# Kernel tuning notes

Measured on AMD Instinct MI355X. Metric: run time of the kernel, lower is better.

## Reference

```python
import jax, jax.numpy as jnp
import numpy as np

B, N, D, P = 16, 128, 1024, 128  # batch, seq_len, n_in, n_mlp
SCALE = 0  # scores divided by P**SCALE (supar convention); scale=0 => no-op


def setup_inputs() -> dict:
    key = jax.random.key(0)
    ks = jax.random.split(key, 6)
    s_in = 1.0 / np.sqrt(D)   # keep MLP activations ~unit scale
    s_w = 1.0 / P             # keep triple-product scores bounded
    return {
        "x": jax.random.normal(ks[0], (B, N, D), jnp.float32),
        "x_span": jax.random.normal(ks[1], (B, N, D), jnp.float32),
        # MLP projections (Linear weight stored torch-style as (out, in))
        "Wx": jax.random.normal(ks[2], (P, D), jnp.float32) * s_in,
        "bx": jnp.zeros((P,), jnp.float32),
        "Wy": jax.random.normal(ks[3], (P, D), jnp.float32) * s_in,
        "by": jnp.zeros((P,), jnp.float32),
        "Wz": jax.random.normal(ks[4], (P, D), jnp.float32) * s_in,
        "bz": jnp.zeros((P,), jnp.float32),
        # Triaffine weight: (P+1 [bias_x], P [z, no bias], P+1 [bias_y]), n_out=1 squeezed
        "W3": jax.random.normal(ks[5], (P + 1, P, P + 1), jnp.float32) * s_w,
    }


def _mlp(h, W, b):
    # supar MLP: Linear + LeakyReLU(0.1); dropout=0 at inference
    return jax.nn.leaky_relu(h @ W.T + b, 0.1)


def reference(x, x_span, Wx, bx, Wy, by, Wz, bz, W3):
    xp = _mlp(x_span, Wx, bx)  # (B,N,P)  -> triaffine arg x
    yp = _mlp(x_span, Wy, by)  # (B,N,P)  -> triaffine arg y
    zp = _mlp(x, Wz, bz)       # (B,N,P)  -> triaffine arg z (head words)
    ones = jnp.ones((B, N, 1), xp.dtype)
    x1 = jnp.concatenate([xp, ones], axis=-1)  # bias_x
    y1 = jnp.concatenate([yp, ones], axis=-1)  # bias_y
    # w: per-head-word bilinear map, (B,N,P+1,P+1)
    w = jnp.einsum('bzk,ikj->bzij', zp, W3)
    # s: (B, z, x, y) = (B,N,N,N)
    s = jnp.einsum('bxi,bzij,byj->bzxy', x1, w, y1)
    s = s / (P ** SCALE)
    # Span2oScorer: s.permute(0, 2, 3, 1).float() -> (B, span_i, span_j, head)
    return jnp.transpose(s, (0, 2, 3, 1)).astype(jnp.float32)
```

## Files before the change

### kernel.cpp

```cpp
#include <hip/hip_runtime.h>

typedef __bf16 bf16;
typedef __bf16 bf16x8 __attribute__((ext_vector_type(8)));
typedef __bf16 bf16x4 __attribute__((ext_vector_type(4)));
typedef float f32x4 __attribute__((ext_vector_type(4)));

#define MFMA(a, b, c) __builtin_amdgcn_mfma_f32_16x16x32_bf16((a), (b), (c), 0, 0, 0)

static __device__ __forceinline__ f32x4 zero4() {
    f32x4 z; z[0] = 0.f; z[1] = 0.f; z[2] = 0.f; z[3] = 0.f; return z;
}

__global__ __launch_bounds__(256) void k_prep(
    const float* __restrict__ x, const float* __restrict__ xsp,
    const float* __restrict__ Wx, const float* __restrict__ Wy, const float* __restrict__ Wz,
    const float* __restrict__ W3,
    bf16* __restrict__ xb, bf16* __restrict__ xspb, bf16* __restrict__ wbf,
    bf16* __restrict__ w3b, float* __restrict__ w3bias)
{
    const int b = blockIdx.x, t = threadIdx.x;
    if (b < 1120) {
        const float* src; bf16* dst; int base;
        if (b < 512)       { src = xsp; dst = xspb; base = b * 4096; }
        else if (b < 1024) { src = x;   dst = xb;   base = (b - 512) * 4096; }
        else {
            int i = b - 1024;
            int proj = i >> 5;
            src = (proj == 0) ? Wx : (proj == 1) ? Wy : Wz;
            dst = wbf + proj * 131072;
            base = (i & 31) * 4096;
        }
        int o = base + t * 16;
#pragma unroll
        for (int u = 0; u < 4; u++) {
            float4 v = *(const float4*)(src + o + u * 4);
            bf16x4 w; w[0] = (bf16)v.x; w[1] = (bf16)v.y; w[2] = (bf16)v.z; w[3] = (bf16)v.w;
            *(bf16x4*)(dst + o + u * 4) = w;
        }
    } else {
        int nb = b - 1120;
        int n = nb * 8 + (t >> 5);
        int c = t & 31;
        const float* row = W3 + n * 129;
        bf16x4 w;
        w[0] = (bf16)row[4 * c + 0];
        w[1] = (bf16)row[4 * c + 1];
        w[2] = (bf16)row[4 * c + 2];
        w[3] = (bf16)row[4 * c + 3];
        *(bf16x4*)(w3b + n * 136 + 4 * c) = w;
        if (c == 0) w3bias[n] = row[128];
    }
}

__global__ __launch_bounds__(256) void k_mlp(
    const bf16* __restrict__ xspb, const bf16* __restrict__ xb,
    const bf16* __restrict__ wbf,
    const float* __restrict__ bx, const float* __restrict__ by, const float* __restrict__ bz,
    bf16* __restrict__ pout)
{
    const int proj = blockIdx.y;
    const bf16* A = (proj == 2) ? xb : xspb;
    const bf16* W = wbf + proj * 131072;
    const float* bias = (proj == 0) ? bx : (proj == 1) ? by : bz;
    bf16* out = pout + proj * 262144;

    const int tid = threadIdx.x;
    const int wv = tid >> 6, lane = tid & 63, quad = lane >> 4, lr = lane & 15;
    const int m0 = blockIdx.x * 16;

    f32x4 acc[2];
    acc[0] = zero4(); acc[1] = zero4();

    const bf16* brow = A + (m0 + lr) * 1024 + quad * 8;
    const bf16* arow = W + (wv * 16 + lr) * 1024 + quad * 8;

#pragma unroll 4
    for (int kw = 0; kw < 32; kw++) {
        bf16x8 bfr = *(const bf16x8*)(brow + kw * 32);
        bf16x8 a0 = *(const bf16x8*)(arow + kw * 32);
        bf16x8 a1 = *(const bf16x8*)(arow + 65536 + kw * 32);
        acc[0] = MFMA(a0, bfr, acc[0]);
        acc[1] = MFMA(a1, bfr, acc[1]);
    }
#pragma unroll
    for (int s = 0; s < 2; s++) {
        int p = (wv + s * 4) * 16 + quad * 4;
        float4 bv = *(const float4*)(bias + p);
        int m = m0 + lr;
        bf16x4 o;
        float v0 = acc[s][0] + bv.x; o[0] = (bf16)(v0 > 0.f ? v0 : 0.1f * v0);
        float v1 = acc[s][1] + bv.y; o[1] = (bf16)(v1 > 0.f ? v1 : 0.1f * v1);
        float v2 = acc[s][2] + bv.z; o[2] = (bf16)(v2 > 0.f ? v2 : 0.1f * v2);
        float v3 = acc[s][3] + bv.w; o[3] = (bf16)(v3 > 0.f ? v3 : 0.1f * v3);
        *(bf16x4*)(out + m * 128 + p) = o;
    }
}

__global__ __launch_bounds__(256, 4) void k_vgemm(
    const bf16* __restrict__ yp,
    const bf16* __restrict__ w3b,
    const float* __restrict__ w3bias,
    bf16* __restrict__ V)
{
    __shared__ bf16 Vt[128 * 136];
    const int b = blockIdx.y;
    const int n0 = blockIdx.x * 128;
    const int tid = threadIdx.x;
    const int wv = tid >> 6, lane = tid & 63, quad = lane >> 4, lr = lane & 15;
    const int y0 = wv * 32;

    const bf16* Ab = yp + b * 16384;

    f32x4 acc[8][2];
#pragma unroll
    for (int nt = 0; nt < 8; nt++) { acc[nt][0] = zero4(); acc[nt][1] = zero4(); }

#pragma unroll
    for (int kw = 0; kw < 4; kw++) {
        bf16x8 b0 = *(const bf16x8*)(Ab + (y0 + lr) * 128 + kw * 32 + quad * 8);
        bf16x8 b1 = *(const bf16x8*)(Ab + (y0 + 16 + lr) * 128 + kw * 32 + quad * 8);
#pragma unroll
        for (int nt = 0; nt < 8; nt++) {
            bf16x8 af = *(const bf16x8*)(w3b + (n0 + nt * 16 + lr) * 136 + kw * 32 + quad * 8);
            acc[nt][0] = MFMA(af, b0, acc[nt][0]);
            acc[nt][1] = MFMA(af, b1, acc[nt][1]);
        }
    }
#pragma unroll
    for (int nt = 0; nt < 8; nt++) {
        int nl = nt * 16 + quad * 4;
        float4 bv = *(const float4*)(w3bias + n0 + nl);
#pragma unroll
        for (int s = 0; s < 2; s++) {
            int y = y0 + s * 16 + lr;
            bf16x4 o;
            o[0] = (bf16)(acc[nt][s][0] + bv.x);
            o[1] = (bf16)(acc[nt][s][1] + bv.y);
            o[2] = (bf16)(acc[nt][s][2] + bv.z);
            o[3] = (bf16)(acc[nt][s][3] + bv.w);
            *(bf16x4*)(&Vt[y * 136 + nl]) = o;
        }
    }
    __syncthreads();
    const int yr = tid >> 4, nn = (tid & 15) * 8;
#pragma unroll
    for (int pass = 0; pass < 8; pass++) {
        int y = pass * 16 + yr;
        bf16x8 v = *(const bf16x8*)(&Vt[y * 136 + nn]);
        *(bf16x8*)(V + (b * 128 + y) * 16512 + n0 + nn) = v;
    }
}

__global__ __launch_bounds__(512, 4) void k_score(
    const bf16* __restrict__ xp,
    const bf16* __restrict__ zp,
    const bf16* __restrict__ V,
    float* __restrict__ out)
{
    __shared__ __align__(16) bf16 Vl[129 * 136];
    __shared__ float Hb[128];
    const int bi = blockIdx.x;
    const int b = bi >> 7, y = bi & 127;
    const int tid = threadIdx.x;
    const int wv = tid >> 6, lane = tid & 63, quad = lane >> 4, lr = lane & 15;
    const int r0 = wv * 16 + lr;

    const bf16* Zb = zp + b * 16384;
    const bf16* Xb = xp + b * 16384;
    const bf16* Vby = V + (b * 128 + y) * 16512;

    bf16x8 st[4];
#pragma unroll
    for (int u = 0; u < 4; u++) st[u] = *(const bf16x8*)(Vby + (tid + u * 512) * 8);
    bf16x8 st4;
#pragma unroll
    for (int q = 0; q < 8; q++) st4[q] = (bf16)0.f;
    if (tid < 16) st4 = *(const bf16x8*)(Vby + (2048 + tid) * 8);

    bf16x8 bz[4];
#pragma unroll
    for (int kw = 0; kw < 4; kw++) bz[kw] = *(const bf16x8*)(Zb + r0 * 128 + kw * 32 + quad * 8);

#pragma unroll
    for (int u = 0; u < 4; u++) {
        int c = tid + u * 512;
        *(bf16x8*)(&Vl[(c >> 4) * 136 + (c & 15) * 8]) = st[u];
    }
    if (tid < 16) *(bf16x8*)(&Vl[128 * 136 + tid * 8]) = st4;
    __syncthreads();

    f32x4 acc1[9];
#pragma unroll
    for (int it = 0; it < 9; it++) acc1[it] = zero4();

#pragma unroll
    for (int kw = 0; kw < 4; kw++) {
#pragma unroll
        for (int it = 0; it < 8; it++) {
            bf16x8 af = *(const bf16x8*)(&Vl[(it * 16 + lr) * 136 + kw * 32 + quad * 8]);
            acc1[it] = MFMA(af, bz[kw], acc1[it]);
        }
        bf16x8 a8;
#pragma unroll
        for (int q = 0; q < 8; q++) a8[q] = (bf16)0.f;
        if (lr == 0) a8 = *(const bf16x8*)(&Vl[128 * 136 + kw * 32 + quad * 8]);
        acc1[8] = MFMA(a8, bz[kw], acc1[8]);
    }
    __syncthreads();

    bf16x8 bxf[4];
#pragma unroll
    for (int iw = 0; iw < 4; iw++) bxf[iw] = *(const bf16x8*)(Xb + r0 * 128 + iw * 32 + quad * 8);

#pragma unroll
    for (int it = 0; it < 8; it++) {
        int i = it * 16 + quad * 4;
        bf16x4 o;
        o[0] = (bf16)acc1[it][0];
        o[1] = (bf16)acc1[it][1];
        o[2] = (bf16)acc1[it][2];
        o[3] = (bf16)acc1[it][3];
        *(bf16x4*)(&Vl[r0 * 136 + i]) = o;
    }
    if (quad == 0) Hb[r0] = acc1[8][0];
    __syncthreads();

    f32x4 acc2[8];
#pragma unroll
    for (int zt = 0; zt < 8; zt++) acc2[zt] = zero4();

#pragma unroll
    for (int iw = 0; iw < 4; iw++) {
#pragma unroll
        for (int zt = 0; zt < 8; zt++) {
            bf16x8 ah = *(const bf16x8*)(&Vl[(zt * 16 + lr) * 136 + iw * 32 + quad * 8]);
            acc2[zt] = MFMA(ah, bxf[iw], acc2[zt]);
        }
    }
#pragma unroll
    for (int zt = 0; zt < 8; zt++) {
        int zb = zt * 16 + quad * 4;
        f32x4 hb = *(const f32x4*)(&Hb[zb]);
        int xx = r0;
        f32x4 o;
        o[0] = acc2[zt][0] + hb[0];
        o[1] = acc2[zt][1] + hb[1];
        o[2] = acc2[zt][2] + hb[2];
        o[3] = acc2[zt][3] + hb[3];
        *(f32x4*)(out + (((b * 128 + xx) * 128 + y) * 128 + zb)) = o;
    }
}

extern "C" void kernel_launch(void* const* d_in, const int* in_sizes, int n_in,
                              void* d_out, int out_size, void* d_ws, size_t ws_size,
                              hipStream_t stream) {
    const float* x   = (const float*)d_in[0];
    const float* xsp = (const float*)d_in[1];
    const float* Wx  = (const float*)d_in[2];
    const float* bx  = (const float*)d_in[3];
    const float* Wy  = (const float*)d_in[4];
    const float* by  = (const float*)d_in[5];
    const float* Wz  = (const float*)d_in[6];
    const float* bz  = (const float*)d_in[7];
    const float* W3  = (const float*)d_in[8];
    float* out = (float*)d_out;

    char* ws = (char*)d_ws;
    bf16*  xspb   = (bf16*)(ws);
    bf16*  xb     = (bf16*)(ws + 4194304);
    bf16*  wbf    = (bf16*)(ws + 8388608);
    bf16*  w3b    = (bf16*)(ws + 9175040);
    bf16*  pout   = (bf16*)(ws + 13666304);
    bf16*  V      = (bf16*)(ws + 15239168);
    float* w3bias = (float*)(ws + 82872320);

    k_prep<<<3184, 256, 0, stream>>>(x, xsp, Wx, Wy, Wz, W3, xb, xspb, wbf, w3b, w3bias);
    k_mlp<<<dim3(128, 3), 256, 0, stream>>>(xspb, xb, wbf, bx, by, bz, pout);
    k_vgemm<<<dim3(129, 16), 256, 0, stream>>>(pout + 262144 , w3b, w3bias, V);
    k_score<<<2048, 512, 0, stream>>>(pout , pout + 524288 , V, out);
}
```

Baseline: 251.6 us.

## Process four y slices per block with double-buffered V prefetch in score kernel

k_score now handles four consecutive y values per block instead of one, cutting the grid from 2048 to 512 blocks. The Z and X fragments are loaded once and reused across all four slices. The next V slice is fetched into registers and written to a second LDS buffer while the current slice is in its MFMA phase. This is meant to hide global load latency and amortise per-block setup, but it doubles LDS use (about 70 KB per block), which lowers occupancy, and the smaller grid may underfill the 256 CUs.

```diff
diff --git a/kernel.cpp b/kernel.cpp
--- a/kernel.cpp
+++ b/kernel.cpp
@@ -157,97 +157,120 @@
     const bf16* __restrict__ V,
     float* __restrict__ out)
 {
-    __shared__ __align__(16) bf16 Vl[129 * 136];
+    __shared__ __align__(16) bf16 Vl[2][129 * 136];
     __shared__ float Hb[128];
-    const int bi = blockIdx.x;
-    const int b = bi >> 7, y = bi & 127;
     const int tid = threadIdx.x;
     const int wv = tid >> 6, lane = tid & 63, quad = lane >> 4, lr = lane & 15;
     const int r0 = wv * 16 + lr;
 
+    const int it0 = blockIdx.x * 4;
+    const int b = it0 >> 7;
+    const int y0 = it0 & 127;
+
     const bf16* Zb = zp + b * 16384;
     const bf16* Xb = xp + b * 16384;
-    const bf16* Vby = V + (b * 128 + y) * 16512;
+    const bf16* Vbase = V + (b * 128 + y0) * 16512;
 
     bf16x8 st[4];
 #pragma unroll
-    for (int u = 0; u < 4; u++) st[u] = *(const bf16x8*)(Vby + (tid + u * 512) * 8);
+    for (int u = 0; u < 4; u++) st[u] = *(const bf16x8*)(Vbase + (tid + u * 512) * 8);
     bf16x8 st4;
 #pragma unroll
     for (int q = 0; q < 8; q++) st4[q] = (bf16)0.f;
-    if (tid < 16) st4 = *(const bf16x8*)(Vby + (2048 + tid) * 8);
-
-    bf16x8 bz[4];
+    if (tid < 16) st4 = *(const bf16x8*)(Vbase + (2048 + tid) * 8);
+
+    bf16x8 bz[4], bxf[4];
 #pragma unroll
     for (int kw = 0; kw < 4; kw++) bz[kw] = *(const bf16x8*)(Zb + r0 * 128 + kw * 32 + quad * 8);
+#pragma unroll
+    for (int iw = 0; iw < 4; iw++) bxf[iw] = *(const bf16x8*)(Xb + r0 * 128 + iw * 32 + quad * 8);
 
 #pragma unroll
     for (int u = 0; u < 4; u++) {
         int c = tid + u * 512;
-        *(bf16x8*)(&Vl[(c >> 4) * 136 + (c & 15) * 8]) = st[u];
-    }
-    if (tid < 16) *(bf16x8*)(&Vl[128 * 136 + tid * 8]) = st4;
-    __syncthreads();
-
-    f32x4 acc1[9];
-#pragma unroll
-    for (int it = 0; it < 9; it++) acc1[it] = zero4();
-
-#pragma unroll
-    for (int kw = 0; kw < 4; kw++) {
+        *(bf16x8*)(&Vl[0][(c >> 4) * 136 + (c & 15) * 8]) = st[u];
+    }
+    if (tid < 16) *(bf16x8*)(&Vl[0][128 * 136 + tid * 8]) = st4;
+
+#pragma unroll 1
+    for (int n = 0; n < 4; n++) {
+        const int cb = n & 1;
+        const bf16* Vc = &Vl[cb][0];
+        bf16* Vn = &Vl[cb ^ 1][0];
+
+        if (n < 3) {
+            const bf16* Vnx = Vbase + (n + 1) * 16512;
+#pragma unroll
+            for (int u = 0; u < 4; u++) st[u] = *(const bf16x8*)(Vnx + (tid + u * 512) * 8);
+            if (tid < 16) st4 = *(const bf16x8*)(Vnx + (2048 + tid) * 8);
+        }
+        __syncthreads();
+
+        f32x4 acc1[9];
+#pragma unroll
+        for (int it = 0; it < 9; it++) acc1[it] = zero4();
+
+#pragma unroll
+        for (int kw = 0; kw < 4; kw++) {
+#pragma unroll
+            for (int it = 0; it < 8; it++) {
+                bf16x8 af = *(const bf16x8*)(Vc + (it * 16 + lr) * 136 + kw * 32 + quad * 8);
+                acc1[it] = MFMA(af, bz[kw], acc1[it]);
+            }
+            bf16x8 a8;
+#pragma unroll
+            for (int q = 0; q < 8; q++) a8[q] = (bf16)0.f;
+            if (lr == 0) a8 = *(const bf16x8*)(Vc + 128 * 136 + kw * 32 + quad * 8);
+            acc1[8] = MFMA(a8, bz[kw], acc1[8]);
+        }
+
+        if (n < 3) {
+#pragma unroll
+            for (int u = 0; u < 4; u++) {
+                int c = tid + u * 512;
+                *(bf16x8*)(Vn + (c >> 4) * 136 + (c & 15) * 8) = st[u];
+            }
+            if (tid < 16) *(bf16x8*)(Vn + 128 * 136 + tid * 8) = st4;
+        }
+        __syncthreads();
+
+        bf16* Hc = &Vl[cb][0];
 #pragma unroll
         for (int it = 0; it < 8; it++) {
-            bf16x8 af = *(const bf16x8*)(&Vl[(it * 16 + lr) * 136 + kw * 32 + quad * 8]);
-            acc1[it] = MFMA(af, bz[kw], acc1[it]);
-        }
-        bf16x8 a8;
-#pragma unroll
-        for (int q = 0; q < 8; q++) a8[q] = (bf16)0.f;
-        if (lr == 0) a8 = *(const bf16x8*)(&Vl[128 * 136 + kw * 32 + quad * 8]);
-        acc1[8] = MFMA(a8, bz[kw], acc1[8]);
-    }
-    __syncthreads();
-
-    bf16x8 bxf[4];
-#pragma unroll
-    for (int iw = 0; iw < 4; iw++) bxf[iw] = *(const bf16x8*)(Xb + r0 * 128 + iw * 32 + quad * 8);
-
-#pragma unroll
-    for (int it = 0; it < 8; it++) {
-        int i = it * 16 + quad * 4;
-        bf16x4 o;
-        o[0] = (bf16)acc1[it][0];
-        o[1] = (bf16)acc1[it][1];
-        o[2] = (bf16)acc1[it][2];
-        o[3] = (bf16)acc1[it][3];
-        *(bf16x4*)(&Vl[r0 * 136 + i]) = o;
-    }
-    if (quad == 0) Hb[r0] = acc1[8][0];
-    __syncthreads();
-
-    f32x4 acc2[8];
-#pragma unroll
-    for (int zt = 0; zt < 8; zt++) acc2[zt] = zero4();
-
-#pragma unroll
-    for (int iw = 0; iw < 4; iw++) {
+            int i = it * 16 + quad * 4;
+            bf16x4 o;
+            o[0] = (bf16)acc1[it][0];
+            o[1] = (bf16)acc1[it][1];
+            o[2] = (bf16)acc1[it][2];
+            o[3] = (bf16)acc1[it][3];
+            *(bf16x4*)(Hc + r0 * 136 + i) = o;
+        }
+        if (quad == 0) Hb[r0] = acc1[8][0];
+        __syncthreads();
+
+        f32x4 acc2[8];
+#pragma unroll
+        for (int zt = 0; zt < 8; zt++) acc2[zt] = zero4();
+
+#pragma unroll
+        for (int iw = 0; iw < 4; iw++) {
+#pragma unroll
+            for (int zt = 0; zt < 8; zt++) {
+                bf16x8 ah = *(const bf16x8*)(Hc + (zt * 16 + lr) * 136 + iw * 32 + quad * 8);
+                acc2[zt] = MFMA(ah, bxf[iw], acc2[zt]);
+            }
+        }
 #pragma unroll
         for (int zt = 0; zt < 8; zt++) {
-            bf16x8 ah = *(const bf16x8*)(&Vl[(zt * 16 + lr) * 136 + iw * 32 + quad * 8]);
-            acc2[zt] = MFMA(ah, bxf[iw], acc2[zt]);
-        }
-    }
-#pragma unroll
-    for (int zt = 0; zt < 8; zt++) {
-        int zb = zt * 16 + quad * 4;
-        f32x4 hb = *(const f32x4*)(&Hb[zb]);
-        int xx = r0;
-        f32x4 o;
-        o[0] = acc2[zt][0] + hb[0];
-        o[1] = acc2[zt][1] + hb[1];
-        o[2] = acc2[zt][2] + hb[2];
-        o[3] = acc2[zt][3] + hb[3];
-        *(f32x4*)(out + (((b * 128 + xx) * 128 + y) * 128 + zb)) = o;
+            int zb = zt * 16 + quad * 4;
+            f32x4 hb = *(const f32x4*)(&Hb[zb]);
+            f32x4 o;
+            o[0] = acc2[zt][0] + hb[0];
+            o[1] = acc2[zt][1] + hb[1];
+            o[2] = acc2[zt][2] + hb[2];
+            o[3] = acc2[zt][3] + hb[3];
+            *(f32x4*)(out + (((b * 128 + r0) * 128 + (y0 + n)) * 128 + zb)) = o;
+        }
     }
 }
 
@@ -277,5 +300,5 @@
     k_prep<<<3184, 256, 0, stream>>>(x, xsp, Wx, Wy, Wz, W3, xb, xspb, wbf, w3b, w3bias);
     k_mlp<<<dim3(128, 3), 256, 0, stream>>>(xspb, xb, wbf, bx, by, bz, pout);
     k_vgemm<<<dim3(129, 16), 256, 0, stream>>>(pout + 262144 , w3b, w3bias, V);
-    k_score<<<2048, 512, 0, stream>>>(pout , pout + 524288 , V, out);
-}
+    k_score<<<512, 512, 0, stream>>>(pout , pout + 524288 , V, out);
+}
```

Result: no change. 254.1 us (+1.0%).
